# Optimization experiments

Measured on AMD Instinct MI355X. Metric: run time of the kernel, lower is better.

The kernel has to match this reference:

```python
import jax, jax.numpy as jnp
import numpy as np

B, S, HID = 1, 2048, 2048
H, KV, D = 16, 4, 128  # head_dim = HID // H; GQA group size g = H // KV
THETA = 10000.0


def setup_inputs() -> dict:
    key = jax.random.key(0)
    ks = jax.random.split(key, 5)
    s = 0.02  # initializer_range
    return {
        "hidden_states": jax.random.normal(ks[0], (B, S, HID), jnp.float32),
        "wq": jax.random.normal(ks[1], (HID, H * D), jnp.float32) * s,
        "wk": jax.random.normal(ks[2], (HID, KV * D), jnp.float32) * s,
        "wv": jax.random.normal(ks[3], (HID, KV * D), jnp.float32) * s,
        "wo": jax.random.normal(ks[4], (H * D, HID), jnp.float32) * s,
        "attention_mask": jnp.ones((B, S), jnp.int32),
        "position_ids": jnp.broadcast_to(jnp.arange(S, dtype=jnp.int32), (B, S)),
    }


def _rope(x, position_ids):
    # x: [b, s, h, d]; rotate consecutive (even, odd) pairs by angle t * theta^{-2j/d}
    half = D // 2
    inv_freq = 1.0 / (THETA ** (jnp.arange(0, D, 2, dtype=jnp.float32) / D))  # [half]
    ang = position_ids[..., None].astype(jnp.float32) * inv_freq  # [b, s, half]
    cos = jnp.cos(ang)[:, :, None, :]  # [b, s, 1, half]
    sin = jnp.sin(ang)[:, :, None, :]
    xr = x.astype(jnp.float32).reshape(*x.shape[:-1], half, 2)
    x0, x1 = xr[..., 0], xr[..., 1]
    out = jnp.stack((x0 * cos - x1 * sin, x0 * sin + x1 * cos), axis=-1)
    return out.reshape(x.shape)


def reference(hidden_states, wq, wk, wv, wo, attention_mask, position_ids):
    b, s, _ = hidden_states.shape
    g = H // KV
    xq = (hidden_states @ wq).reshape(b, s, H, D)
    xk = (hidden_states @ wk).reshape(b, s, KV, D)
    xv = (hidden_states @ wv).reshape(b, s, KV, D)
    # GQA: each kv head repeated g consecutive times -> H heads (matches einops '(h g)')
    xk = jnp.repeat(xk, g, axis=2)
    xv = jnp.repeat(xv, g, axis=2)
    xq = _rope(xq, position_ids)
    xk = _rope(xk, position_ids)
    # causal + padding mask -> additive bias (0 or -inf), softmax in fp32
    causal = jnp.tril(jnp.ones((s, s), dtype=bool))[None, None]  # [1,1,q,k]
    mask = causal & (attention_mask[:, None, None, :] > 0)  # [b,1,q,k]
    scores = jnp.einsum('bqhd,bkhd->bhqk', xq.astype(jnp.float32), xk.astype(jnp.float32))
    scores = scores / jnp.sqrt(jnp.float32(D))
    scores = jnp.where(mask, scores, jnp.finfo(jnp.float32).min)
    attn_weights = jax.nn.softmax(scores, axis=-1)  # [b,h,q,k] fp32
    attn = jnp.einsum('bhqk,bkhd->bqhd', attn_weights, xv.astype(jnp.float32))
    return (attn.reshape(b, s, H * D).astype(hidden_states.dtype)) @ wo
```

## Files before the change

### kernel.cpp

```cpp
#include <hip/hip_runtime.h>
#include <hip/hip_bf16.h>

#define S_LEN 2048
#define HIDDIM 2048
#define NH 16
#define NKV 4
#define HD 128
#define KVROW 1024
#define QKVN 3072

typedef __attribute__((ext_vector_type(8))) short short8;
typedef __attribute__((ext_vector_type(8))) unsigned short ushort8;
typedef __attribute__((ext_vector_type(4))) unsigned short ushort4v;
typedef __attribute__((ext_vector_type(4))) float f32x4;

__device__ __forceinline__ unsigned short f2bf(float f) {
  union { float f; unsigned int u; } v; v.f = f;
  unsigned int r = (v.u + 0x7FFFu + ((v.u >> 16) & 1u)) >> 16;
  return (unsigned short)r;
}
__device__ __forceinline__ float bf2f(unsigned short h) {
  union { unsigned int u; float f; } v; v.u = ((unsigned int)h) << 16;
  return v.f;
}

__device__ __forceinline__ void gl2lds16(const unsigned short* src,
                                         unsigned short* dst) {
  __builtin_amdgcn_global_load_lds(
      (const __attribute__((address_space(1))) unsigned int*)src,
      (__attribute__((address_space(3))) unsigned int*)dst, 16, 0, 0);
}

__global__ __launch_bounds__(256) void h2b_kernel(const float* __restrict__ H,
                                                  unsigned short* __restrict__ Hb) {
  int i = (blockIdx.x * 256 + threadIdx.x) * 8;
  float4 a = *(const float4*)(H + i), b = *(const float4*)(H + i + 4);
  ushort8 r;
  r[0] = f2bf(a.x); r[1] = f2bf(a.y); r[2] = f2bf(a.z); r[3] = f2bf(a.w);
  r[4] = f2bf(b.x); r[5] = f2bf(b.y); r[6] = f2bf(b.z); r[7] = f2bf(b.w);
  *(ushort8*)(Hb + i) = r;
}

__global__ __launch_bounds__(256) void transpose_w(
    const float* __restrict__ W, unsigned short* __restrict__ Wt,
    int Nsrc, int Kdst, int n_off) {
  __shared__ unsigned short Ts[64][72];
  const int n0 = blockIdx.x * 64, k0 = blockIdx.y * 64;
  const int tid = threadIdx.x;
  const int c2 = (tid & 31) * 2, rb = tid >> 5;
#pragma unroll
  for (int p = 0; p < 8; ++p) {
    int r = rb + p * 8;
    float2 v = *(const float2*)&W[(size_t)(k0 + r) * Nsrc + n0 + c2];
    Ts[c2][r] = f2bf(v.x);
    Ts[c2 + 1][r] = f2bf(v.y);
  }
  __syncthreads();
  const int n = tid >> 2, kq = (tid & 3) * 16;
  ushort8 w0 = *(const ushort8*)&Ts[n][kq];
  ushort8 w1 = *(const ushort8*)&Ts[n][kq + 8];
  size_t base = (size_t)(n_off + n0 + n) * Kdst + k0 + kq;
  *(ushort8*)&Wt[base] = w0;
  *(ushort8*)&Wt[base + 8] = w1;
}

__global__ __launch_bounds__(256) void transpose_v(
    const unsigned short* __restrict__ KVb, unsigned short* __restrict__ Vt) {
  __shared__ unsigned short Ts[64][72];
  const int c0 = blockIdx.x * 64, s0 = blockIdx.y * 64;
  const int tid = threadIdx.x;
  const int sr = tid >> 2, cq = (tid & 3) * 16;
  ushort8 a = *(const ushort8*)&KVb[(size_t)(s0 + sr) * KVROW + 512 + c0 + cq];
  ushort8 b = *(const ushort8*)&KVb[(size_t)(s0 + sr) * KVROW + 512 + c0 + cq + 8];
#pragma unroll
  for (int j = 0; j < 8; ++j) { Ts[cq + j][sr] = a[j]; Ts[cq + 8 + j][sr] = b[j]; }
  __syncthreads();
  const int c = tid >> 2, sq = (tid & 3) * 16;
  ushort8 w0 = *(const ushort8*)&Ts[c][sq];
  ushort8 w1 = *(const ushort8*)&Ts[c][sq + 8];
  *(ushort8*)&Vt[(size_t)(c0 + c) * S_LEN + s0 + sq] = w0;
  *(ushort8*)&Vt[(size_t)(c0 + c) * S_LEN + s0 + sq + 8] = w1;
}

template <bool CF>
__global__ __launch_bounds__(256) void gemm_tn(
    const unsigned short* __restrict__ A, const unsigned short* __restrict__ Bt,
    void* __restrict__ C1, void* __restrict__ C2,
    int M, int N, int K, int splitcol, int ld1, int ld2) {
  __shared__ unsigned short As[2][128 * 64];
  __shared__ unsigned short Bs[2][64 * 64];
  const int m0 = blockIdx.y * 128, n0 = blockIdx.x * 64;
  const int tid = threadIdx.x, wid = tid >> 6, lane = tid & 63;
  const int wr = wid >> 1, wc = wid & 1;
  const int lr = lane & 15, lg = lane >> 4;

  f32x4 acc[4][2];
#pragma unroll
  for (int m = 0; m < 4; ++m)
#pragma unroll
    for (int n = 0; n < 2; ++n) acc[m][n] = (f32x4){0.f, 0.f, 0.f, 0.f};

  const int srow = lane >> 3;
  const int scolb = (lane & 7) << 4;
  auto stage = [&](int k0, int b) {
#pragma unroll
    for (int j = 0; j < 4; ++j) {
      int row = wid * 32 + j * 8 + srow;
      int src = (scolb ^ ((row & 7) << 4)) >> 1;
      gl2lds16(A + (size_t)(m0 + row) * K + k0 + src,
               &As[b][(wid * 32 + j * 8) * 64]);
    }
#pragma unroll
    for (int j = 0; j < 2; ++j) {
      int row = wid * 16 + j * 8 + srow;
      int src = (scolb ^ ((row & 7) << 4)) >> 1;
      gl2lds16(Bt + (size_t)(n0 + row) * K + k0 + src,
               &Bs[b][(wid * 16 + j * 8) * 64]);
    }
  };

  stage(0, 0);
  int cur = 0;
  for (int k0 = 0; k0 < K; k0 += 64) {
    __syncthreads();
    if (k0 + 64 < K) stage(k0 + 64, cur ^ 1);
#pragma unroll
    for (int s = 0; s < 2; ++s) {
      short8 af[4], bfv[2];
#pragma unroll
      for (int m = 0; m < 4; ++m) {
        int row = wr * 64 + m * 16 + lr;
        int off = ((s * 64 + lg * 16) ^ ((row & 7) << 4)) >> 1;
        af[m] = *(const short8*)&As[cur][row * 64 + off];
      }
#pragma unroll
      for (int n = 0; n < 2; ++n) {
        int row = wc * 32 + n * 16 + lr;
        int off = ((s * 64 + lg * 16) ^ ((row & 7) << 4)) >> 1;
        bfv[n] = *(const short8*)&Bs[cur][row * 64 + off];
      }
#pragma unroll
      for (int m = 0; m < 4; ++m)
#pragma unroll
        for (int n = 0; n < 2; ++n)
          acc[m][n] = __builtin_amdgcn_mfma_f32_16x16x32_bf16(af[m], bfv[n], acc[m][n], 0, 0, 0);
    }
    cur ^= 1;
  }

#pragma unroll
  for (int m = 0; m < 4; ++m)
#pragma unroll
    for (int n = 0; n < 2; ++n)
#pragma unroll
      for (int r = 0; r < 4; ++r) {
        int row = m0 + wr * 64 + m * 16 + lg * 4 + r;
        int col = n0 + wc * 32 + n * 16 + lr;
        float v = acc[m][n][r];
        if (CF) ((float*)C1)[(size_t)row * ld1 + col] = v;
        else if (col < splitcol) ((unsigned short*)C1)[(size_t)row * ld1 + col] = f2bf(v);
        else ((unsigned short*)C2)[(size_t)row * ld2 + (col - splitcol)] = f2bf(v);
      }
}

__global__ void rope2(unsigned short* __restrict__ Q,
                      unsigned short* __restrict__ KV,
                      const int* __restrict__ pos) {
  int idx = blockIdx.x * blockDim.x + threadIdx.x;
  if (idx >= S_LEN * 64) return;
  int s = idx >> 6, j = idx & 63;
  float inv = exp2f(-0.2076205059304703f * (float)j);
  float ang = (float)pos[s] * inv;
  float sn, cs;
  __sincosf(ang, &sn, &cs);
  auto rot = [&](unsigned short* base) {
    unsigned* p = (unsigned*)base;
    unsigned v = *p;
    float x0 = bf2f((unsigned short)(v & 0xffff));
    float x1 = bf2f((unsigned short)(v >> 16));
    unsigned r = (unsigned)f2bf(x0 * cs - x1 * sn) |
                 ((unsigned)f2bf(x0 * sn + x1 * cs) << 16);
    *p = r;
  };
#pragma unroll
  for (int hh = 0; hh < NH; ++hh) rot(Q + (size_t)s * HIDDIM + hh * HD + 2 * j);
#pragma unroll
  for (int hh = 0; hh < NKV; ++hh) rot(KV + (size_t)s * KVROW + hh * HD + 2 * j);
}

__global__ void maskbits_kernel(const int* __restrict__ amask,
                                unsigned* __restrict__ mb) {
  int w = threadIdx.x;
  unsigned m = 0;
#pragma unroll
  for (int b = 0; b < 32; ++b) m |= (amask[w * 32 + b] != 0 ? 1u : 0u) << b;
  mb[w] = m;
}

__global__ __launch_bounds__(256) void attn_kernel(
    const unsigned short* __restrict__ Qb, const unsigned short* __restrict__ KVb,
    const unsigned short* __restrict__ VtG, const unsigned* __restrict__ mbits,
    unsigned short* __restrict__ Ob,
    unsigned short* __restrict__ Opart, float* __restrict__ Lpart, int nsplit) {
  const int x = (int)blockIdx.x;
  const int qt = 63 - (x >> 2);
  const int c = x & 3;
  const int kvh = (int)blockIdx.y;
  const int nch = (qt >> 4) + 1;
  if (nsplit == 0) { if (c != 0) return; }
  else if (c >= nch) return;
  const int qb = qt * 32;
  int kbeg = 0, kend = qb + 32;
  bool partial = false;
  if (nsplit && nch > 1) {
    kbeg = c * 512;
    kend = min(kend, kbeg + 512);
    partial = true;
  }

  __shared__ unsigned short Klds[2][32 * 128];
  __shared__ unsigned short Vlds[2][128 * 32];
  __shared__ unsigned short Plds[4][32][40];
  const int tid = threadIdx.x, wid = tid >> 6, lane = tid & 63;
  const int lr = lane & 15, lg = lane >> 4;
  const int h = kvh * 4 + wid;

  short8 qfa[4], qfb[4];
  {
    const unsigned short* qpa = Qb + (size_t)(qb + lr) * HIDDIM + h * HD;
    const unsigned short* qpb = Qb + (size_t)(qb + 16 + lr) * HIDDIM + h * HD;
#pragma unroll
    for (int cc = 0; cc < 4; ++cc) {
      qfa[cc] = *(const short8*)(qpa + cc * 32 + lg * 8);
      qfb[cc] = *(const short8*)(qpb + cc * 32 + lg * 8);
    }
  }
  f32x4 oa[8], ob[8];
#pragma unroll
  for (int cc = 0; cc < 8; ++cc) {
    oa[cc] = (f32x4){0.f, 0.f, 0.f, 0.f};
    ob[cc] = (f32x4){0.f, 0.f, 0.f, 0.f};
  }
  float lsa = 0.f, lsb = 0.f;

  const unsigned short* Vg = VtG + (size_t)(kvh * HD) * S_LEN;

  const int ksr_ = lane >> 4;
  const int kscb = (lane & 15) << 4;
  const int vsr_ = lane >> 2;
  const int vscb = (lane & 3) << 4;

  auto stage = [&](int kt, int b) {
#pragma unroll
    for (int j = 0; j < 2; ++j) {
      int krow = wid * 8 + j * 4 + ksr_;
      int ksrc = (kscb ^ ((krow & 7) << 4)) >> 1;
      gl2lds16(KVb + (size_t)(kt + krow) * KVROW + kvh * HD + ksrc,
               &Klds[b][(wid * 8 + j * 4) * 128]);
      int vrow = wid * 32 + j * 16 + vsr_;
      int vsrc = (vscb ^ ((vrow & 3) << 4)) >> 1;
      gl2lds16(Vg + (size_t)vrow * S_LEN + kt + vsrc,
               &Vlds[b][(wid * 32 + j * 16) * 32]);
    }
  };

  stage(kbeg, 0);

  const int qra = qb + lr, qrb = qb + 16 + lr;
  const float SCALE = 0.08838834764831845f;
  int cur = 0;

  for (int kt = kbeg; kt < kend; kt += 32) {
    __syncthreads();
    if (kt + 32 < kend) stage(kt + 32, cur ^ 1);

    f32x4 sa[2], sb[2];
#pragma unroll
    for (int t = 0; t < 2; ++t) {
      sa[t] = (f32x4){0.f, 0.f, 0.f, 0.f};
      sb[t] = (f32x4){0.f, 0.f, 0.f, 0.f};
    }
    const unsigned short* kbase = &Klds[cur][0];
    __builtin_amdgcn_s_setprio(1);
#pragma unroll
    for (int t = 0; t < 2; ++t)
#pragma unroll
      for (int cc = 0; cc < 4; ++cc) {
        short8 kf = *(const short8*)(kbase + ((t * 16 + lr) << 7) +
                                     ((((cc << 6) + (lg << 4)) ^ ((lr & 7) << 4)) >> 1));
        sa[t] = __builtin_amdgcn_mfma_f32_16x16x32_bf16(kf, qfa[cc], sa[t], 0, 0, 0);
        sb[t] = __builtin_amdgcn_mfma_f32_16x16x32_bf16(kf, qfb[cc], sb[t], 0, 0, 0);
      }
    __builtin_amdgcn_s_setprio(0);
    const unsigned mw = mbits[kt >> 5];
    float pa[2][4], pb[2][4];
    if ((kt + 31 <= qb) && (mw == ~0u)) {
#pragma unroll
      for (int t = 0; t < 2; ++t)
#pragma unroll
        for (int r = 0; r < 4; ++r) {
          float va = __expf(sa[t][r] * SCALE - 3.0f);
          float vb = __expf(sb[t][r] * SCALE - 3.0f);
          pa[t][r] = va; lsa += va;
          pb[t][r] = vb; lsb += vb;
        }
    } else {
#pragma unroll
      for (int t = 0; t < 2; ++t)
#pragma unroll
        for (int r = 0; r < 4; ++r) {
          int kk = t * 16 + lg * 4 + r;
          bool okm = (mw >> kk) & 1u;
          float va = __expf((okm && kt + kk <= qra) ? sa[t][r] * SCALE - 3.0f : -1e30f);
          float vb = __expf((okm && kt + kk <= qrb) ? sb[t][r] * SCALE - 3.0f : -1e30f);
          pa[t][r] = va; lsa += va;
          pb[t][r] = vb; lsb += vb;
        }
    }
#pragma unroll
    for (int t = 0; t < 2; ++t) {
      ushort4v pka, pkb;
#pragma unroll
      for (int r = 0; r < 4; ++r) { pka[r] = f2bf(pa[t][r]); pkb[r] = f2bf(pb[t][r]); }
      *(ushort4v*)&Plds[wid][lr][t * 16 + lg * 4] = pka;
      *(ushort4v*)&Plds[wid][16 + lr][t * 16 + lg * 4] = pkb;
    }
    short8 pfa = *(const short8*)&Plds[wid][lr][lg * 8];
    short8 pfb = *(const short8*)&Plds[wid][16 + lr][lg * 8];
    const unsigned short* vbase = &Vlds[cur][0];
    __builtin_amdgcn_s_setprio(1);
#pragma unroll
    for (int cc = 0; cc < 8; ++cc) {
      short8 vf = *(const short8*)(vbase + ((cc * 16 + lr) << 5) +
                                   ((lg ^ (lr & 3)) << 3));
      oa[cc] = __builtin_amdgcn_mfma_f32_16x16x32_bf16(pfa, vf, oa[cc], 0, 0, 0);
      ob[cc] = __builtin_amdgcn_mfma_f32_16x16x32_bf16(pfb, vf, ob[cc], 0, 0, 0);
    }
    __builtin_amdgcn_s_setprio(0);
    cur ^= 1;
  }

  float la = lsa;
  la += __shfl_xor(la, 16, 64);
  la += __shfl_xor(la, 32, 64);
  float lb = lsb;
  lb += __shfl_xor(lb, 16, 64);
  lb += __shfl_xor(lb, 32, 64);

  if (!partial) {
    float lra[4], lrb[4];
#pragma unroll
    for (int r = 0; r < 4; ++r) {
      lra[r] = 1.0f / __shfl(la, lg * 4 + r, 16);
      lrb[r] = 1.0f / __shfl(lb, lg * 4 + r, 16);
    }
#pragma unroll
    for (int cc = 0; cc < 8; ++cc)
#pragma unroll
      for (int r = 0; r < 4; ++r) {
        const int rowa = qb + lg * 4 + r;
        const int rowb = qb + 16 + lg * 4 + r;
        Ob[(size_t)rowa * HIDDIM + h * HD + cc * 16 + lr] = f2bf(oa[cc][r] * lra[r]);
        Ob[(size_t)rowb * HIDDIM + h * HD + cc * 16 + lr] = f2bf(ob[cc][r] * lrb[r]);
      }
  } else {
    const int g = qt >> 4, j = qt & 15;
    const int base = (g == 1) ? 0 : (g == 2) ? 32 : 80;
    const int slot = base + j * nch + c + 144 * kvh;
    if (lg == 0) {
      Lpart[slot * 128 + wid * 32 + lr] = la;
      Lpart[slot * 128 + wid * 32 + 16 + lr] = lb;
    }
#pragma unroll
    for (int cc = 0; cc < 8; ++cc)
#pragma unroll
      for (int r = 0; r < 4; ++r) {
        Opart[(size_t)slot * 16384 + wid * 4096 +
              (lg * 4 + r) * 128 + cc * 16 + lr] = f2bf(oa[cc][r]);
        Opart[(size_t)slot * 16384 + wid * 4096 +
              (16 + lg * 4 + r) * 128 + cc * 16 + lr] = f2bf(ob[cc][r]);
      }
  }
}

__global__ __launch_bounds__(256) void combine_kernel(
    const unsigned short* __restrict__ Opart, const float* __restrict__ Lpart,
    unsigned short* __restrict__ Ab) {
  const int qt = 16 + (int)blockIdx.x;
  const int kvh = (int)blockIdx.y;
  const int nch = (qt >> 4) + 1;
  const int g = qt >> 4, j = qt & 15;
  const int base = (g == 1) ? 0 : (g == 2) ? 32 : 80;
  const int s0 = base + j * nch + 144 * kvh;
  const int tid = threadIdx.x;
  const int rowid = tid >> 1;
  const int d0 = (tid & 1) * 64;
  float L = 0.f;
  for (int cc = 0; cc < nch; ++cc) L += Lpart[(s0 + cc) * 128 + rowid];
  const float linv = 1.0f / L;
  const int h = kvh * 4 + (rowid >> 5);
  const int row = qt * 32 + (rowid & 31);
  unsigned short* dst = Ab + (size_t)row * HIDDIM + h * HD + d0;
  for (int i = 0; i < 64; i += 8) {
    float acc[8] = {0, 0, 0, 0, 0, 0, 0, 0};
    for (int cc = 0; cc < nch; ++cc) {
      ushort8 v = *(const ushort8*)&Opart[(size_t)(s0 + cc) * 16384 +
                                          rowid * 128 + d0 + i];
#pragma unroll
      for (int k = 0; k < 8; ++k) acc[k] += bf2f(v[k]);
    }
    ushort8 r;
#pragma unroll
    for (int k = 0; k < 8; ++k) r[k] = f2bf(acc[k] * linv);
    *(ushort8*)(dst + i) = r;
  }
}

extern "C" void kernel_launch(void* const* d_in, const int* in_sizes, int n_in,
                              void* d_out, int out_size, void* d_ws, size_t ws_size,
                              hipStream_t stream) {
  const float* hidden = (const float*)d_in[0];
  const float* wq = (const float*)d_in[1];
  const float* wk = (const float*)d_in[2];
  const float* wv = (const float*)d_in[3];
  const float* wo = (const float*)d_in[4];
  const int* amask = (const int*)d_in[5];
  const int* pos = (const int*)d_in[6];

  unsigned short* Qb = (unsigned short*)d_ws;
  unsigned short* KVb = Qb + (size_t)S_LEN * HIDDIM;
  unsigned short* Ab = KVb + (size_t)S_LEN * KVROW;
  unsigned short* WT1 = Ab + (size_t)S_LEN * HIDDIM;
  unsigned short* Hb = WT1 + (size_t)QKVN * HIDDIM;
  float* out = (float*)d_out;

  unsigned short* Opart = WT1;
  unsigned short* Vt_chunk = WT1 + (size_t)576 * 16384;
  unsigned* mbits_chunk = (unsigned*)((char*)d_ws + 41943040ull);
  float* Lpart = (float*)((char*)d_ws + 41943296ull);
  const size_t need_chunk = 42238208ull;
  unsigned short* Vt_fb = WT1 + (size_t)HIDDIM * HIDDIM;
  unsigned* mbits_fb = (unsigned*)((char*)d_ws + 31457280ull);

  const int nsplit = (ws_size >= need_chunk) ? 1 : 0;
  unsigned short* Vt = nsplit ? Vt_chunk : Vt_fb;
  unsigned* mbits = nsplit ? mbits_chunk : mbits_fb;

  dim3 blk(256);
  h2b_kernel<<<2048, blk, 0, stream>>>(hidden, Hb);
  transpose_w<<<dim3(32, 32), blk, 0, stream>>>(wq, WT1, HIDDIM, HIDDIM, 0);
  transpose_w<<<dim3(8, 32), blk, 0, stream>>>(wk, WT1, 512, HIDDIM, 2048);
  transpose_w<<<dim3(8, 32), blk, 0, stream>>>(wv, WT1, 512, HIDDIM, 2560);
  gemm_tn<false><<<dim3(QKVN / 64, S_LEN / 128), blk, 0, stream>>>(
      Hb, WT1, Qb, KVb, S_LEN, QKVN, HIDDIM, 2048, HIDDIM, KVROW);
  transpose_v<<<dim3(8, 32), blk, 0, stream>>>(KVb, Vt);
  rope2<<<(S_LEN * 64 + 255) / 256, blk, 0, stream>>>(Qb, KVb, pos);
  maskbits_kernel<<<1, 64, 0, stream>>>(amask, mbits);
  attn_kernel<<<dim3(256, NKV), blk, 0, stream>>>(
      Qb, KVb, Vt, mbits, Ab, Opart, Lpart, nsplit);
  if (nsplit)
    combine_kernel<<<dim3(48, NKV), blk, 0, stream>>>(Opart, Lpart, Ab);
  transpose_w<<<dim3(32, 32), blk, 0, stream>>>(wo, WT1, HIDDIM, HIDDIM, 0);
  gemm_tn<true><<<dim3(HIDDIM / 64, S_LEN / 128), blk, 0, stream>>>(
      Ab, WT1, out, nullptr, S_LEN, HIDDIM, HIDDIM, HIDDIM, HIDDIM, 0);
}
```

Baseline: 170.5 us.

## Merge prep launches and replace LDS P round-trip with wave shuffles

Merges the hidden-state bf16 conversion, the Q/K/V weight transposes and the mask-bit packing into one prep kernel. The V transpose and RoPE now share a single launch as well. This removes several small kernel launches and their gaps. Inside attention, the softmax probabilities are moved from the MFMA output layout to the input layout with cross-lane shuffles instead of an LDS write/read, freeing shared memory and avoiding LDS traffic at the cost of extra shuffle instructions.

```diff
diff --git a/kernel.cpp b/kernel.cpp
--- a/kernel.cpp
+++ b/kernel.cpp
@@ -11,7 +11,6 @@
 
 typedef __attribute__((ext_vector_type(8))) short short8;
 typedef __attribute__((ext_vector_type(8))) unsigned short ushort8;
-typedef __attribute__((ext_vector_type(4))) unsigned short ushort4v;
 typedef __attribute__((ext_vector_type(4))) float f32x4;
 
 __device__ __forceinline__ unsigned short f2bf(float f) {
@@ -31,22 +30,11 @@
       (__attribute__((address_space(3))) unsigned int*)dst, 16, 0, 0);
 }
 
-__global__ __launch_bounds__(256) void h2b_kernel(const float* __restrict__ H,
-                                                  unsigned short* __restrict__ Hb) {
-  int i = (blockIdx.x * 256 + threadIdx.x) * 8;
-  float4 a = *(const float4*)(H + i), b = *(const float4*)(H + i + 4);
-  ushort8 r;
-  r[0] = f2bf(a.x); r[1] = f2bf(a.y); r[2] = f2bf(a.z); r[3] = f2bf(a.w);
-  r[4] = f2bf(b.x); r[5] = f2bf(b.y); r[6] = f2bf(b.z); r[7] = f2bf(b.w);
-  *(ushort8*)(Hb + i) = r;
-}
-
-__global__ __launch_bounds__(256) void transpose_w(
+__device__ __forceinline__ void tw_body(
     const float* __restrict__ W, unsigned short* __restrict__ Wt,
-    int Nsrc, int Kdst, int n_off) {
-  __shared__ unsigned short Ts[64][72];
-  const int n0 = blockIdx.x * 64, k0 = blockIdx.y * 64;
-  const int tid = threadIdx.x;
+    int Nsrc, int Kdst, int n_off, int bx, int by, int tid,
+    unsigned short (*Ts)[72]) {
+  const int n0 = bx * 64, k0 = by * 64;
   const int c2 = (tid & 31) * 2, rb = tid >> 5;
 #pragma unroll
   for (int p = 0; p < 8; ++p) {
@@ -64,22 +52,86 @@
   *(ushort8*)&Wt[base + 8] = w1;
 }
 
-__global__ __launch_bounds__(256) void transpose_v(
-    const unsigned short* __restrict__ KVb, unsigned short* __restrict__ Vt) {
+__global__ __launch_bounds__(256) void prep_kernel(
+    const float* __restrict__ H, unsigned short* __restrict__ Hb,
+    const float* __restrict__ wq, const float* __restrict__ wk,
+    const float* __restrict__ wv, unsigned short* __restrict__ WT1,
+    const int* __restrict__ amask, unsigned* __restrict__ mb) {
   __shared__ unsigned short Ts[64][72];
-  const int c0 = blockIdx.x * 64, s0 = blockIdx.y * 64;
-  const int tid = threadIdx.x;
-  const int sr = tid >> 2, cq = (tid & 3) * 16;
-  ushort8 a = *(const ushort8*)&KVb[(size_t)(s0 + sr) * KVROW + 512 + c0 + cq];
-  ushort8 b = *(const ushort8*)&KVb[(size_t)(s0 + sr) * KVROW + 512 + c0 + cq + 8];
-#pragma unroll
-  for (int j = 0; j < 8; ++j) { Ts[cq + j][sr] = a[j]; Ts[cq + 8 + j][sr] = b[j]; }
-  __syncthreads();
-  const int c = tid >> 2, sq = (tid & 3) * 16;
-  ushort8 w0 = *(const ushort8*)&Ts[c][sq];
-  ushort8 w1 = *(const ushort8*)&Ts[c][sq + 8];
-  *(ushort8*)&Vt[(size_t)(c0 + c) * S_LEN + s0 + sq] = w0;
-  *(ushort8*)&Vt[(size_t)(c0 + c) * S_LEN + s0 + sq + 8] = w1;
+  const int b = (int)blockIdx.x, tid = threadIdx.x;
+  if (b < 2048) {
+    int i = (b * 256 + tid) * 8;
+    float4 a = *(const float4*)(H + i), c = *(const float4*)(H + i + 4);
+    ushort8 r;
+    r[0] = f2bf(a.x); r[1] = f2bf(a.y); r[2] = f2bf(a.z); r[3] = f2bf(a.w);
+    r[4] = f2bf(c.x); r[5] = f2bf(c.y); r[6] = f2bf(c.z); r[7] = f2bf(c.w);
+    *(ushort8*)(Hb + i) = r;
+  } else if (b < 3072) {
+    int t = b - 2048;
+    tw_body(wq, WT1, HIDDIM, HIDDIM, 0, t & 31, t >> 5, tid, Ts);
+  } else if (b < 3328) {
+    int t = b - 3072;
+    tw_body(wk, WT1, 512, HIDDIM, 2048, t & 7, t >> 3, tid, Ts);
+  } else if (b < 3584) {
+    int t = b - 3328;
+    tw_body(wv, WT1, 512, HIDDIM, 2560, t & 7, t >> 3, tid, Ts);
+  } else {
+    if (tid < 64) {
+      unsigned m = 0;
+#pragma unroll
+      for (int i = 0; i < 32; ++i) m |= (amask[tid * 32 + i] != 0 ? 1u : 0u) << i;
+      mb[tid] = m;
+    }
+  }
+}
+
+__global__ __launch_bounds__(256) void transpose_w(
+    const float* __restrict__ W, unsigned short* __restrict__ Wt,
+    int Nsrc, int Kdst, int n_off) {
+  __shared__ unsigned short Ts[64][72];
+  tw_body(W, Wt, Nsrc, Kdst, n_off, (int)blockIdx.x, (int)blockIdx.y,
+          (int)threadIdx.x, Ts);
+}
+
+__global__ __launch_bounds__(256) void tvrope_kernel(
+    unsigned short* __restrict__ Qb, unsigned short* __restrict__ KVb,
+    unsigned short* __restrict__ Vt, const int* __restrict__ pos) {
+  __shared__ unsigned short Ts[64][72];
+  const int b = (int)blockIdx.x, tid = threadIdx.x;
+  if (b < 256) {
+    const int c0 = (b & 7) * 64, s0 = (b >> 3) * 64;
+    const int sr = tid >> 2, cq = (tid & 3) * 16;
+    ushort8 a = *(const ushort8*)&KVb[(size_t)(s0 + sr) * KVROW + 512 + c0 + cq];
+    ushort8 c = *(const ushort8*)&KVb[(size_t)(s0 + sr) * KVROW + 512 + c0 + cq + 8];
+#pragma unroll
+    for (int j = 0; j < 8; ++j) { Ts[cq + j][sr] = a[j]; Ts[cq + 8 + j][sr] = c[j]; }
+    __syncthreads();
+    const int cc = tid >> 2, sq = (tid & 3) * 16;
+    ushort8 w0 = *(const ushort8*)&Ts[cc][sq];
+    ushort8 w1 = *(const ushort8*)&Ts[cc][sq + 8];
+    *(ushort8*)&Vt[(size_t)(c0 + cc) * S_LEN + s0 + sq] = w0;
+    *(ushort8*)&Vt[(size_t)(c0 + cc) * S_LEN + s0 + sq + 8] = w1;
+  } else {
+    int idx = (b - 256) * 256 + tid;
+    int s = idx >> 6, j = idx & 63;
+    float inv = exp2f(-0.2076205059304703f * (float)j);
+    float ang = (float)pos[s] * inv;
+    float sn, cs;
+    __sincosf(ang, &sn, &cs);
+    auto rot = [&](unsigned short* base) {
+      unsigned* p = (unsigned*)base;
+      unsigned v = *p;
+      float x0 = bf2f((unsigned short)(v & 0xffff));
+      float x1 = bf2f((unsigned short)(v >> 16));
+      unsigned r = (unsigned)f2bf(x0 * cs - x1 * sn) |
+                   ((unsigned)f2bf(x0 * sn + x1 * cs) << 16);
+      *p = r;
+    };
+#pragma unroll
+    for (int hh = 0; hh < NH; ++hh) rot(Qb + (size_t)s * HIDDIM + hh * HD + 2 * j);
+#pragma unroll
+    for (int hh = 0; hh < NKV; ++hh) rot(KVb + (size_t)s * KVROW + hh * HD + 2 * j);
+  }
 }
 
 template <bool CF>
@@ -161,40 +213,6 @@
         else if (col < splitcol) ((unsigned short*)C1)[(size_t)row * ld1 + col] = f2bf(v);
         else ((unsigned short*)C2)[(size_t)row * ld2 + (col - splitcol)] = f2bf(v);
       }
-}
-
-__global__ void rope2(unsigned short* __restrict__ Q,
-                      unsigned short* __restrict__ KV,
-                      const int* __restrict__ pos) {
-  int idx = blockIdx.x * blockDim.x + threadIdx.x;
-  if (idx >= S_LEN * 64) return;
-  int s = idx >> 6, j = idx & 63;
-  float inv = exp2f(-0.2076205059304703f * (float)j);
-  float ang = (float)pos[s] * inv;
-  float sn, cs;
-  __sincosf(ang, &sn, &cs);
-  auto rot = [&](unsigned short* base) {
-    unsigned* p = (unsigned*)base;
-    unsigned v = *p;
-    float x0 = bf2f((unsigned short)(v & 0xffff));
-    float x1 = bf2f((unsigned short)(v >> 16));
-    unsigned r = (unsigned)f2bf(x0 * cs - x1 * sn) |
-                 ((unsigned)f2bf(x0 * sn + x1 * cs) << 16);
-    *p = r;
-  };
-#pragma unroll
-  for (int hh = 0; hh < NH; ++hh) rot(Q + (size_t)s * HIDDIM + hh * HD + 2 * j);
-#pragma unroll
-  for (int hh = 0; hh < NKV; ++hh) rot(KV + (size_t)s * KVROW + hh * HD + 2 * j);
-}
-
-__global__ void maskbits_kernel(const int* __restrict__ amask,
-                                unsigned* __restrict__ mb) {
-  int w = threadIdx.x;
-  unsigned m = 0;
-#pragma unroll
-  for (int b = 0; b < 32; ++b) m |= (amask[w * 32 + b] != 0 ? 1u : 0u) << b;
-  mb[w] = m;
 }
 
 __global__ __launch_bounds__(256) void attn_kernel(
@@ -220,7 +238,6 @@
 
   __shared__ unsigned short Klds[2][32 * 128];
   __shared__ unsigned short Vlds[2][128 * 32];
-  __shared__ unsigned short Plds[4][32][40];
   const int tid = threadIdx.x, wid = tid >> 6, lane = tid & 63;
   const int lr = lane & 15, lg = lane >> 4;
   const int h = kvh * 4 + wid;
@@ -270,6 +287,26 @@
   const float SCALE = 0.08838834764831845f;
   int cur = 0;
 
+  const int s0 = lr + ((lg & 1) << 5);
+  const int s1 = s0 + 16;
+  const bool lo = (lg < 2);
+  auto exchange = [&](const float p[2][4]) -> short8 {
+    unsigned W0 = (unsigned)f2bf(p[0][0]) | ((unsigned)f2bf(p[0][1]) << 16);
+    unsigned W1 = (unsigned)f2bf(p[0][2]) | ((unsigned)f2bf(p[0][3]) << 16);
+    unsigned W2 = (unsigned)f2bf(p[1][0]) | ((unsigned)f2bf(p[1][1]) << 16);
+    unsigned W3 = (unsigned)f2bf(p[1][2]) | ((unsigned)f2bf(p[1][3]) << 16);
+    unsigned x0 = __shfl(W0, s0, 64), y0 = __shfl(W2, s0, 64);
+    unsigned x1 = __shfl(W1, s0, 64), y1 = __shfl(W3, s0, 64);
+    unsigned x2 = __shfl(W0, s1, 64), y2 = __shfl(W2, s1, 64);
+    unsigned x3 = __shfl(W1, s1, 64), y3 = __shfl(W3, s1, 64);
+    union { unsigned u[4]; short8 s8; } pu;
+    pu.u[0] = lo ? x0 : y0;
+    pu.u[1] = lo ? x1 : y1;
+    pu.u[2] = lo ? x2 : y2;
+    pu.u[3] = lo ? x3 : y3;
+    return pu.s8;
+  };
+
   for (int kt = kbeg; kt < kend; kt += 32) {
     __syncthreads();
     if (kt + 32 < kend) stage(kt + 32, cur ^ 1);
@@ -317,16 +354,8 @@
           pb[t][r] = vb; lsb += vb;
         }
     }
-#pragma unroll
-    for (int t = 0; t < 2; ++t) {
-      ushort4v pka, pkb;
-#pragma unroll
-      for (int r = 0; r < 4; ++r) { pka[r] = f2bf(pa[t][r]); pkb[r] = f2bf(pb[t][r]); }
-      *(ushort4v*)&Plds[wid][lr][t * 16 + lg * 4] = pka;
-      *(ushort4v*)&Plds[wid][16 + lr][t * 16 + lg * 4] = pkb;
-    }
-    short8 pfa = *(const short8*)&Plds[wid][lr][lg * 8];
-    short8 pfb = *(const short8*)&Plds[wid][16 + lr][lg * 8];
+    short8 pfa = exchange(pa);
+    short8 pfb = exchange(pb);
     const unsigned short* vbase = &Vlds[cur][0];
     __builtin_amdgcn_s_setprio(1);
 #pragma unroll
@@ -447,15 +476,10 @@
   unsigned* mbits = nsplit ? mbits_chunk : mbits_fb;
 
   dim3 blk(256);
-  h2b_kernel<<<2048, blk, 0, stream>>>(hidden, Hb);
-  transpose_w<<<dim3(32, 32), blk, 0, stream>>>(wq, WT1, HIDDIM, HIDDIM, 0);
-  transpose_w<<<dim3(8, 32), blk, 0, stream>>>(wk, WT1, 512, HIDDIM, 2048);
-  transpose_w<<<dim3(8, 32), blk, 0, stream>>>(wv, WT1, 512, HIDDIM, 2560);
+  prep_kernel<<<3585, blk, 0, stream>>>(hidden, Hb, wq, wk, wv, WT1, amask, mbits);
   gemm_tn<false><<<dim3(QKVN / 64, S_LEN / 128), blk, 0, stream>>>(
       Hb, WT1, Qb, KVb, S_LEN, QKVN, HIDDIM, 2048, HIDDIM, KVROW);
-  transpose_v<<<dim3(8, 32), blk, 0, stream>>>(KVb, Vt);
-  rope2<<<(S_LEN * 64 + 255) / 256, blk, 0, stream>>>(Qb, KVb, pos);
-  maskbits_kernel<<<1, 64, 0, stream>>>(amask, mbits);
+  tvrope_kernel<<<768, blk, 0, stream>>>(Qb, KVb, Vt, pos);
   attn_kernel<<<dim3(256, NKV), blk, 0, stream>>>(
       Qb, KVb, Vt, mbits, Ab, Opart, Lpart, nsplit);
   if (nsplit)
```

Result: faster. 162.3 us (-4.8%).
